# Performance work log

Measured on AMD Instinct MI355X. Metric: run time of the kernel, lower is better.

The kernel has to match this reference:

```python
import jax, jax.numpy as jnp
import numpy as np

D_MODEL = 768
D_HID = 3072
D_OUT = 768
N_EXP = 8
TOP_K = 2
B, S = 2, 2048
LN_EPS = 1e-5


def setup_inputs() -> dict:
    key = jax.random.key(0)
    ks = jax.random.split(key, 10)
    sc_in = 1.0 / np.sqrt(D_MODEL)
    sc_hid = 1.0 / np.sqrt(D_HID)
    return {
        "x": jax.random.normal(ks[0], (B, S, D_MODEL), dtype=jnp.float32),
        "Wr": jax.random.normal(ks[1], (D_MODEL, N_EXP), dtype=jnp.float32) * sc_in,
        "br": jnp.zeros((N_EXP,), dtype=jnp.float32),
        "W1": jax.random.normal(ks[2], (N_EXP, D_MODEL, D_HID), dtype=jnp.float32) * sc_in,
        "b1": jnp.zeros((N_EXP, D_HID), dtype=jnp.float32),
        "W2": jax.random.normal(ks[3], (N_EXP, D_HID, D_OUT), dtype=jnp.float32) * sc_hid,
        "b2": jnp.zeros((N_EXP, D_OUT), dtype=jnp.float32),
        "ln_g": jnp.ones((D_OUT,), dtype=jnp.float32),
        "ln_b": jnp.zeros((D_OUT,), dtype=jnp.float32),
    }


def reference(x, Wr, br, W1, b1, W2, b2, ln_g, ln_b):
    # --- top-k router ---
    logits = jnp.einsum("bsd,de->bse", x, Wr) + br          # [B,S,E]
    probs = jax.nn.softmax(logits, axis=-1)
    top_vals, top_idx = jax.lax.top_k(probs, TOP_K)          # [B,S,K]
    routing_weights = top_vals / jnp.sum(top_vals, axis=-1, keepdims=True)

    # per-token weight given to each expert (0 if not selected)
    onehot = jax.nn.one_hot(top_idx, N_EXP, dtype=x.dtype)   # [B,S,K,E]
    expert_weights = jnp.einsum("bsk,bske->bse", routing_weights, onehot)

    # --- dense per-expert FFN over ALL tokens (faithful to source loop) ---
    h = jax.nn.gelu(jnp.einsum("bsd,edh->besh", x, W1) + b1[None, :, None, :])
    y = jnp.einsum("besh,eho->beso", h, W2) + b2[None, :, None, :]  # [B,E,S,O]

    # weighted combine
    out = jnp.einsum("beso,bse->bso", y, expert_weights)     # [B,S,O]

    # --- output LayerNorm ---
    mu = jnp.mean(out, axis=-1, keepdims=True)
    var = jnp.mean(jnp.square(out - mu), axis=-1, keepdims=True)
    out = (out - mu) * jax.lax.rsqrt(var + LN_EPS) * ln_g + ln_b
    return out
```

## Files before the change

kernel.cpp:

```cpp
#include <hip/hip_runtime.h>
#include <hip/hip_bf16.h>

#define TOKENS 4096
#define DMODEL 768
#define DHID   3072
#define NEXP   8
#define MAXT   40

typedef __bf16 bf16x8 __attribute__((ext_vector_type(8)));
typedef float  f32x4  __attribute__((ext_vector_type(4)));
typedef unsigned short ushort_t;

#define VMCNT(n) asm volatile("s_waitcnt vmcnt(" #n ")" ::: "memory")

__device__ __forceinline__ void wg_barrier() {
    asm volatile("" ::: "memory");
    __builtin_amdgcn_s_barrier();
    asm volatile("" ::: "memory");
}

__device__ __forceinline__ float gelu_tanh(float x) {
    float z = 0.7978845608028654f * (x + 0.044715f * x * x * x);
    float t = 1.0f - 2.0f / (__expf(2.0f * z) + 1.0f);
    return 0.5f * x * (1.0f + t);
}

__device__ __forceinline__ float bf2f(ushort_t u) {
    unsigned v = ((unsigned)u) << 16;
    return __builtin_bit_cast(float, v);
}

__device__ __forceinline__ void gload16(const void* g, void* l) {
    __builtin_amdgcn_global_load_lds((const __attribute__((address_space(1))) void*)g,
                                     (__attribute__((address_space(3))) void*)l, 16, 0, 0);
}

__global__ void k_transpose_cvt(const float* __restrict__ in, ushort_t* __restrict__ out,
                                int R, int C) {
    __shared__ float tile[64 * 68];
    const int bx = blockIdx.x, by = blockIdx.y, bz = blockIdx.z;
    const float* ip = in + (size_t)bz * R * C;
    ushort_t* op = out + (size_t)bz * R * C;
    const int tid = threadIdx.x;
    {
        const int cq = tid & 15, rg = tid >> 4;
#pragma unroll
        for (int i = 0; i < 4; ++i) {
            int rl = rg + i * 16;
            float4 v = *(const float4*)(ip + (size_t)(by * 64 + rl) * C + bx * 64 + cq * 4);
            *(float4*)(&tile[rl * 68 + cq * 4]) = v;
        }
    }
    __syncthreads();
    {
        const int rq = tid & 15, cg = tid >> 4;
#pragma unroll
        for (int i = 0; i < 4; ++i) {
            int cl = cg + i * 16;
            ushort4 o;
            o.x = __builtin_bit_cast(ushort_t, (__bf16)tile[(rq * 4 + 0) * 68 + cl]);
            o.y = __builtin_bit_cast(ushort_t, (__bf16)tile[(rq * 4 + 1) * 68 + cl]);
            o.z = __builtin_bit_cast(ushort_t, (__bf16)tile[(rq * 4 + 2) * 68 + cl]);
            o.w = __builtin_bit_cast(ushort_t, (__bf16)tile[(rq * 4 + 3) * 68 + cl]);
            *(ushort4*)(op + (size_t)(bx * 64 + cl) * R + by * 64 + rq * 4) = o;
        }
    }
}

__launch_bounds__(256)
__global__ void k_router(const float* __restrict__ x, const float* __restrict__ Wr,
                         const float* __restrict__ br, int* __restrict__ cnt,
                         int* __restrict__ tok, int* __restrict__ slot,
                         float* __restrict__ wslot, ushort_t* __restrict__ xb) {
    __shared__ float WrT[NEXP * DMODEL];
    __shared__ int   te0[32], te1[32];
    __shared__ int   lcnt[NEXP], gbase[NEXP];

    const int tid = threadIdx.x;
    const int wv = tid >> 6, lane = tid & 63;

#pragma unroll
    for (int i = 0; i < 6; ++i) {
        int idx4 = i * 256 + tid;
        float4 v = ((const float4*)Wr)[idx4];
        int flat = idx4 * 4;
        int d = flat >> 3, e0 = flat & 7;
        WrT[(e0 + 0) * DMODEL + d] = v.x;
        WrT[(e0 + 1) * DMODEL + d] = v.y;
        WrT[(e0 + 2) * DMODEL + d] = v.z;
        WrT[(e0 + 3) * DMODEL + d] = v.w;
    }
    if (tid < NEXP) lcnt[tid] = 0;
    float brv[8];
#pragma unroll
    for (int e = 0; e < 8; ++e) brv[e] = br[e];
    __syncthreads();

#pragma unroll 1
    for (int it = 0; it < 8; ++it) {
        int t = blockIdx.x * 32 + wv * 8 + it;
        const float* xr = x + (size_t)t * DMODEL;
        float4 xv[3];
#pragma unroll
        for (int j = 0; j < 3; ++j) xv[j] = *(const float4*)(xr + (j * 64 + lane) * 4);
#pragma unroll
        for (int j = 0; j < 3; ++j) {
            int base = (j * 64 + lane) * 4;
            ushort4 o;
            o.x = __builtin_bit_cast(ushort_t, (__bf16)xv[j].x);
            o.y = __builtin_bit_cast(ushort_t, (__bf16)xv[j].y);
            o.z = __builtin_bit_cast(ushort_t, (__bf16)xv[j].z);
            o.w = __builtin_bit_cast(ushort_t, (__bf16)xv[j].w);
            *(ushort4*)(xb + (size_t)t * DMODEL + base) = o;
        }
        float lg[8];
#pragma unroll
        for (int e = 0; e < 8; ++e) {
            float s = 0.f;
#pragma unroll
            for (int j = 0; j < 3; ++j) {
                const float4 wv4 = *(const float4*)(&WrT[e * DMODEL + (j * 64 + lane) * 4]);
                s += xv[j].x * wv4.x;
                s += xv[j].y * wv4.y;
                s += xv[j].z * wv4.z;
                s += xv[j].w * wv4.w;
            }
#pragma unroll
            for (int o = 32; o > 0; o >>= 1) s += __shfl_xor(s, o);
            lg[e] = s + brv[e];
        }
        if (lane == 0) {
            int e0 = 0; float b0 = lg[0];
#pragma unroll
            for (int e = 1; e < 8; ++e) if (lg[e] > b0) { b0 = lg[e]; e0 = e; }
            int e1 = -1; float b1v = -1e30f;
#pragma unroll
            for (int e = 0; e < 8; ++e) if (e != e0 && lg[e] > b1v) { b1v = lg[e]; e1 = e; }
            float w0 = 1.f / (1.f + __expf(b1v - b0));
            float w1 = 1.f - w0;
            int lt = wv * 8 + it;
            te0[lt] = e0; te1[lt] = e1;
            wslot[2 * t] = w0; wslot[2 * t + 1] = w1;
        }
    }
    __syncthreads();

    int myE = 0, myPos = 0, myTok = 0, myK = 0;
    if (tid < 64) {
        int lt = tid >> 1; myK = tid & 1;
        myE = myK ? te1[lt] : te0[lt];
        myTok = blockIdx.x * 32 + lt;
        myPos = atomicAdd(&lcnt[myE], 1);
    }
    __syncthreads();
    if (tid < NEXP) gbase[tid] = atomicAdd(&cnt[tid], lcnt[tid]);
    __syncthreads();
    if (tid < 64) {
        int g = gbase[myE] + myPos;
        tok[myE * TOKENS + g] = myTok;
        slot[myE * TOKENS + g] = 2 * myTok + myK;
    }
}

__global__ void k_sched(const int* __restrict__ cnt, int* __restrict__ sch) {
    if (threadIdx.x == 0) {
        int base = 0, n = 0;
        for (int e = 0; e < NEXP; ++e) {
            sch[2 + e] = base;
            int ce = cnt[e];
            for (int m = 0; m < ce; m += 256) sch[16 + n++] = (e << 20) | m;
            base += ce;
        }
        sch[0] = n;
    }
}


#define ISSUE(c, kt1, BOFF)                                                            \
    {                                                                                  \
        _Pragma("unroll")                                                              \
        for (int i_ = 0; i_ < 2; ++i_) {                                               \
            const ushort_t* s_ = (((c) & 1) ? bPtr[i_] : aPtr[i_]) + (kt1) * 64 + (((c) >> 1) * 32); \
            gload16(s_, ldsB + (BOFF) + (((c) & 1) ? 32768 : 0) + (((c) >> 1) * 16384) \
                            + w * 2048 + i_ * 1024);                                   \
        }                                                                              \
    }

#define MFMA32                                                                         \
    __builtin_amdgcn_s_setprio(1);                                                     \
    _Pragma("unroll")                                                                  \
    for (int mi = 0; mi < 8; ++mi) {                                                   \
        _Pragma("unroll")                                                              \
        for (int ni = 0; ni < 4; ++ni)                                                 \
            acc[mi][ni] = __builtin_amdgcn_mfma_f32_16x16x32_bf16(af[mi], bf[ni], acc[mi][ni], 0, 0, 0); \
    }                                                                                  \
    __builtin_amdgcn_s_setprio(0);

#define TILE2(kt, BUFOFF, PF, LAST)                                                    \
    {                                                                                  \
        const char* bufL = ldsB + (BUFOFF);                                            \
        bf16x8 af[8], bf[4];                                                           \
                                                  \
        _Pragma("unroll")                                                              \
        for (int mi = 0; mi < 8; ++mi) af[mi] = *(const bf16x8*)(bufL + abase + mi * 1024); \
        _Pragma("unroll")                                                              \
        for (int ni = 0; ni < 4; ++ni) bf[ni] = *(const bf16x8*)(bufL + bbase + ni * 1024); \
        if (PF) { ISSUE(0, (kt) + 1, (BUFOFF) ^ 65536) ISSUE(1, (kt) + 1, (BUFOFF) ^ 65536) } \
        if (LAST) { VMCNT(0); } else { VMCNT(4); }                                     \
        wg_barrier();                                                                  \
        MFMA32                                                                         \
        wg_barrier();                                                                  \
                                                  \
        _Pragma("unroll")                                                              \
        for (int mi = 0; mi < 8; ++mi) af[mi] = *(const bf16x8*)(bufL + abase + 16384 + mi * 1024); \
        _Pragma("unroll")                                                              \
        for (int ni = 0; ni < 4; ++ni) bf[ni] = *(const bf16x8*)(bufL + bbase + 16384 + ni * 1024); \
        if (PF) { ISSUE(2, (kt) + 1, (BUFOFF) ^ 65536) ISSUE(3, (kt) + 1, (BUFOFF) ^ 65536) \
                  VMCNT(4); }                                                          \
        else    { VMCNT(0); }                                                          \
        wg_barrier();                                                                  \
        MFMA32                                                                         \
        wg_barrier();                                                                  \
    }

template<bool STAGE1>
__launch_bounds__(512, 1)
__global__ void k_gemm8(const ushort_t* __restrict__ Abase, const int* __restrict__ tok,
                        const int* __restrict__ slot, const ushort_t* __restrict__ Wb,
                        const float* __restrict__ bias, void* __restrict__ outp,
                        const int* __restrict__ cnt, const int* __restrict__ sch) {
    constexpr int KR  = STAGE1 ? DMODEL : DHID;
    constexpr int NCn = STAGE1 ? DHID : DMODEL;
    constexpr int NT  = STAGE1 ? (DMODEL / 64) : (DHID / 2 / 64);

    const int bx = blockIdx.x;
    const int tile = (bx & 7) * 5 + (bx >> 3);
    const int nT = sch[0];
    if (tile >= nT) return;
    const int ent = sch[16 + tile];
    const int e = ent >> 20, m0 = ent & 0xFFFFF;
    const int ce = cnt[e];
    const int bH = sch[2 + e];
    const int n0 = blockIdx.y * 256;
    const int kbase = STAGE1 ? 0 : (int)blockIdx.z * (DHID / 2);

    __shared__ ushort_t lds[65536];
    char* ldsB = (char*)lds;

    const int tid = threadIdx.x, lane = tid & 63, w = tid >> 6;
    const int wm = w >> 2, wn = w & 3;
    const int wmBase = wm * 128, wnBase = wn * 64;
    const int fr = lane & 15, fg = lane >> 4;

    const ushort_t* aPtr[2];
    const ushort_t* bPtr[2];
#pragma unroll
    for (int i = 0; i < 2; ++i) {
        int j = w * 2 + i;
        int row = j * 16 + (lane >> 2);
        int gblk = (lane & 3) ^ ((row >> 1) & 3);
        int gi = min(m0 + row, ce - 1);
        size_t ar = STAGE1 ? (size_t)tok[e * TOKENS + gi] : (size_t)(bH + gi);
        aPtr[i] = Abase + ar * KR + kbase + gblk * 8;
        bPtr[i] = Wb + ((size_t)e * NCn + n0 + row) * KR + kbase + gblk * 8;
    }

    const int arow0 = wmBase + fr;
    const int abase = arow0 * 64 + ((fg ^ ((arow0 >> 1) & 3)) << 4);
    const int brow0 = wnBase + fr;
    const int bbase = 32768 + brow0 * 64 + ((fg ^ ((brow0 >> 1) & 3)) << 4);

    f32x4 acc[8][4] = {};

    ISSUE(0, 0, 0) ISSUE(1, 0, 0) ISSUE(2, 0, 0) ISSUE(3, 0, 0)
    VMCNT(4);
    wg_barrier();

#pragma unroll 1
    for (int kt = 0; kt < NT - 2; kt += 2) {
        TILE2(kt, 0, 1, 0)
        TILE2(kt + 1, 65536, 1, 0)
    }
    TILE2(NT - 2, 0, 1, 0)
    TILE2(NT - 1, 65536, 0, 1)

    float bv[4];
#pragma unroll
    for (int ni = 0; ni < 4; ++ni)
        bv[ni] = bias[e * NCn + n0 + wnBase + ni * 16 + fr];
#pragma unroll
    for (int mi = 0; mi < 8; ++mi) {
#pragma unroll
        for (int r4 = 0; r4 < 4; ++r4) {
            int gi = m0 + wmBase + mi * 16 + fg * 4 + r4;
            if (gi < ce) {
                if constexpr (STAGE1) {
                    size_t orow = (size_t)(bH + gi);
#pragma unroll
                    for (int ni = 0; ni < 4; ++ni) {
                        int col = n0 + wnBase + ni * 16 + fr;
                        float v = gelu_tanh(acc[mi][ni][r4] + bv[ni]);
                        ((ushort_t*)outp)[orow * DHID + col] =
                            __builtin_bit_cast(ushort_t, (__bf16)v);
                    }
                } else {
                    size_t orow = (size_t)blockIdx.z * 8192 + (size_t)slot[e * TOKENS + gi];
                    float badd = (blockIdx.z == 0) ? 1.f : 0.f;
#pragma unroll
                    for (int ni = 0; ni < 4; ++ni) {
                        int col = n0 + wnBase + ni * 16 + fr;
                        float v = acc[mi][ni][r4] + badd * bv[ni];
                        ((ushort_t*)outp)[orow * DMODEL + col] =
                            __builtin_bit_cast(ushort_t, (__bf16)v);
                    }
                }
            }
        }
    }
}

__global__ void k_ln(const ushort_t* __restrict__ Y2, const float* __restrict__ wslot,
                     const float* __restrict__ g, const float* __restrict__ b,
                     float* __restrict__ out) {
    int wv = threadIdx.x >> 6, lane = threadIdx.x & 63;
    int t = blockIdx.x * 4 + wv;
    const ushort_t* r00 = Y2 + (size_t)(2 * t) * DMODEL;
    const ushort_t* r01 = Y2 + (size_t)(8192 + 2 * t) * DMODEL;
    const ushort_t* r10 = r00 + DMODEL;
    const ushort_t* r11 = r01 + DMODEL;
    float w0 = wslot[2 * t], w1 = wslot[2 * t + 1];
    float4 v[3];
    float s = 0.f, ss = 0.f;
#pragma unroll
    for (int j = 0; j < 3; ++j) {
        int base = (j * 64 + lane) * 4;
        ushort4 a0 = *(const ushort4*)(r00 + base);
        ushort4 a1 = *(const ushort4*)(r01 + base);
        ushort4 c0 = *(const ushort4*)(r10 + base);
        ushort4 c1 = *(const ushort4*)(r11 + base);
        float4 c;
        c.x = w0 * (bf2f(a0.x) + bf2f(a1.x)) + w1 * (bf2f(c0.x) + bf2f(c1.x));
        c.y = w0 * (bf2f(a0.y) + bf2f(a1.y)) + w1 * (bf2f(c0.y) + bf2f(c1.y));
        c.z = w0 * (bf2f(a0.z) + bf2f(a1.z)) + w1 * (bf2f(c0.z) + bf2f(c1.z));
        c.w = w0 * (bf2f(a0.w) + bf2f(a1.w)) + w1 * (bf2f(c0.w) + bf2f(c1.w));
        v[j] = c;
        s  += c.x + c.y + c.z + c.w;
        ss += c.x * c.x + c.y * c.y + c.z * c.z + c.w * c.w;
    }
#pragma unroll
    for (int o = 32; o > 0; o >>= 1) { s += __shfl_xor(s, o); ss += __shfl_xor(ss, o); }
    float mu = s * (1.f / 768.f);
    float var = ss * (1.f / 768.f) - mu * mu;
    float inv = rsqrtf(var + 1e-5f);
    float* row = out + (size_t)t * DMODEL;
#pragma unroll
    for (int j = 0; j < 3; ++j) {
        int base = (j * 64 + lane) * 4;
        float4 gv = *(const float4*)(g + base);
        float4 bv = *(const float4*)(b + base);
        float4 o4;
        o4.x = (v[j].x - mu) * inv * gv.x + bv.x;
        o4.y = (v[j].y - mu) * inv * gv.y + bv.y;
        o4.z = (v[j].z - mu) * inv * gv.z + bv.z;
        o4.w = (v[j].w - mu) * inv * gv.w + bv.w;
        *(float4*)(row + base) = o4;
    }
}

extern "C" void kernel_launch(void* const* d_in, const int* in_sizes, int n_in,
                              void* d_out, int out_size, void* d_ws, size_t ws_size,
                              hipStream_t stream) {
    const float* x    = (const float*)d_in[0];
    const float* Wr   = (const float*)d_in[1];
    const float* br   = (const float*)d_in[2];
    const float* W1   = (const float*)d_in[3];
    const float* b1   = (const float*)d_in[4];
    const float* W2   = (const float*)d_in[5];
    const float* b2   = (const float*)d_in[6];
    const float* ln_g = (const float*)d_in[7];
    const float* ln_b = (const float*)d_in[8];
    float* out = (float*)d_out;

    char* ws = (char*)d_ws;
    int*      cnt   = (int*)(ws + 0);
    int*      sch   = (int*)(ws + 64);
    int*      tok   = (int*)(ws + 4096);
    int*      slot  = (int*)(ws + 135168);
    float*    wslot = (float*)(ws + 266240);
    ushort_t* xb    = (ushort_t*)(ws + 327680);
    ushort_t* W1t   = (ushort_t*)(ws + 6619136);
    ushort_t* W2t   = (ushort_t*)(ws + 44367872);
    ushort_t* H     = (ushort_t*)(ws + 82116608);
    ushort_t* Y2    = (ushort_t*)(ws + 132448256);

    hipMemsetAsync(cnt, 0, 32, stream);

    k_transpose_cvt<<<dim3(DHID / 64, DMODEL / 64, NEXP), dim3(256), 0, stream>>>(W1, W1t, DMODEL, DHID);
    k_transpose_cvt<<<dim3(DMODEL / 64, DHID / 64, NEXP), dim3(256), 0, stream>>>(W2, W2t, DHID, DMODEL);
    k_router<<<dim3(TOKENS / 32), dim3(256), 0, stream>>>(x, Wr, br, cnt, tok, slot, wslot, xb);
    k_sched<<<dim3(1), dim3(64), 0, stream>>>(cnt, sch);

    k_gemm8<true><<<dim3(MAXT, DHID / 256, 1), dim3(512), 0, stream>>>(
        xb, tok, slot, W1t, b1, H, cnt, sch);
    k_gemm8<false><<<dim3(MAXT, DMODEL / 256, 2), dim3(512), 0, stream>>>(
        H, tok, slot, W2t, b2, Y2, cnt, sch);

    k_ln<<<dim3(TOKENS / 4), dim3(256), 0, stream>>>(Y2, wslot, ln_g, ln_b, out);
}
```

Before: 204.1 us.

## Shrink grouped-GEMM tiles to 128x128 with 256 threads and two blocks per CU

Halves the GEMM block tile from 256x256 to 128x128, uses 4 waves instead of 8, and allows two workgroups per CU. The scheduler now emits 128-row tiles, so MAXT grows to cover the extra tiles. The K-loop is rewritten as a simpler double-buffered loop with one wait per iteration instead of split half-tile prefetches. The intent is more blocks and less padding waste on the ragged expert token counts. The cost is lower data reuse per tile, more global traffic, and a less finely overlapped pipeline.

```diff
diff --git a/kernel.cpp b/kernel.cpp
--- a/kernel.cpp
+++ b/kernel.cpp
@@ -5,7 +5,7 @@
 #define DMODEL 768
 #define DHID   3072
 #define NEXP   8
-#define MAXT   40
+#define MAXT   72
 
 typedef __bf16 bf16x8 __attribute__((ext_vector_type(8)));
 typedef float  f32x4  __attribute__((ext_vector_type(4)));
@@ -168,63 +168,15 @@
         for (int e = 0; e < NEXP; ++e) {
             sch[2 + e] = base;
             int ce = cnt[e];
-            for (int m = 0; m < ce; m += 256) sch[16 + n++] = (e << 20) | m;
+            for (int m = 0; m < ce; m += 128) sch[16 + n++] = (e << 20) | m;
             base += ce;
         }
         sch[0] = n;
     }
 }
 
-
-#define ISSUE(c, kt1, BOFF)                                                            \
-    {                                                                                  \
-        _Pragma("unroll")                                                              \
-        for (int i_ = 0; i_ < 2; ++i_) {                                               \
-            const ushort_t* s_ = (((c) & 1) ? bPtr[i_] : aPtr[i_]) + (kt1) * 64 + (((c) >> 1) * 32); \
-            gload16(s_, ldsB + (BOFF) + (((c) & 1) ? 32768 : 0) + (((c) >> 1) * 16384) \
-                            + w * 2048 + i_ * 1024);                                   \
-        }                                                                              \
-    }
-
-#define MFMA32                                                                         \
-    __builtin_amdgcn_s_setprio(1);                                                     \
-    _Pragma("unroll")                                                                  \
-    for (int mi = 0; mi < 8; ++mi) {                                                   \
-        _Pragma("unroll")                                                              \
-        for (int ni = 0; ni < 4; ++ni)                                                 \
-            acc[mi][ni] = __builtin_amdgcn_mfma_f32_16x16x32_bf16(af[mi], bf[ni], acc[mi][ni], 0, 0, 0); \
-    }                                                                                  \
-    __builtin_amdgcn_s_setprio(0);
-
-#define TILE2(kt, BUFOFF, PF, LAST)                                                    \
-    {                                                                                  \
-        const char* bufL = ldsB + (BUFOFF);                                            \
-        bf16x8 af[8], bf[4];                                                           \
-                                                  \
-        _Pragma("unroll")                                                              \
-        for (int mi = 0; mi < 8; ++mi) af[mi] = *(const bf16x8*)(bufL + abase + mi * 1024); \
-        _Pragma("unroll")                                                              \
-        for (int ni = 0; ni < 4; ++ni) bf[ni] = *(const bf16x8*)(bufL + bbase + ni * 1024); \
-        if (PF) { ISSUE(0, (kt) + 1, (BUFOFF) ^ 65536) ISSUE(1, (kt) + 1, (BUFOFF) ^ 65536) } \
-        if (LAST) { VMCNT(0); } else { VMCNT(4); }                                     \
-        wg_barrier();                                                                  \
-        MFMA32                                                                         \
-        wg_barrier();                                                                  \
-                                                  \
-        _Pragma("unroll")                                                              \
-        for (int mi = 0; mi < 8; ++mi) af[mi] = *(const bf16x8*)(bufL + abase + 16384 + mi * 1024); \
-        _Pragma("unroll")                                                              \
-        for (int ni = 0; ni < 4; ++ni) bf[ni] = *(const bf16x8*)(bufL + bbase + 16384 + ni * 1024); \
-        if (PF) { ISSUE(2, (kt) + 1, (BUFOFF) ^ 65536) ISSUE(3, (kt) + 1, (BUFOFF) ^ 65536) \
-                  VMCNT(4); }                                                          \
-        else    { VMCNT(0); }                                                          \
-        wg_barrier();                                                                  \
-        MFMA32                                                                         \
-        wg_barrier();                                                                  \
-    }
-
 template<bool STAGE1>
-__launch_bounds__(512, 1)
+__launch_bounds__(256, 2)
 __global__ void k_gemm8(const ushort_t* __restrict__ Abase, const int* __restrict__ tok,
                         const int* __restrict__ slot, const ushort_t* __restrict__ Wb,
                         const float* __restrict__ bias, void* __restrict__ outp,
@@ -234,30 +186,29 @@
     constexpr int NT  = STAGE1 ? (DMODEL / 64) : (DHID / 2 / 64);
 
     const int bx = blockIdx.x;
-    const int tile = (bx & 7) * 5 + (bx >> 3);
+    const int tile = (bx & 7) * 9 + (bx >> 3);
     const int nT = sch[0];
     if (tile >= nT) return;
     const int ent = sch[16 + tile];
     const int e = ent >> 20, m0 = ent & 0xFFFFF;
     const int ce = cnt[e];
     const int bH = sch[2 + e];
-    const int n0 = blockIdx.y * 256;
+    const int n0 = blockIdx.y * 128;
     const int kbase = STAGE1 ? 0 : (int)blockIdx.z * (DHID / 2);
 
-    __shared__ ushort_t lds[65536];
+    __shared__ ushort_t lds[32768];
     char* ldsB = (char*)lds;
 
     const int tid = threadIdx.x, lane = tid & 63, w = tid >> 6;
-    const int wm = w >> 2, wn = w & 3;
-    const int wmBase = wm * 128, wnBase = wn * 64;
+    const int wm = w >> 1, wn = w & 1;
+    const int wmBase = wm * 64, wnBase = wn * 64;
     const int fr = lane & 15, fg = lane >> 4;
 
     const ushort_t* aPtr[2];
     const ushort_t* bPtr[2];
 #pragma unroll
     for (int i = 0; i < 2; ++i) {
-        int j = w * 2 + i;
-        int row = j * 16 + (lane >> 2);
+        int row = (w * 2 + i) * 16 + (lane >> 2);
         int gblk = (lane & 3) ^ ((row >> 1) & 3);
         int gi = min(m0 + row, ce - 1);
         size_t ar = STAGE1 ? (size_t)tok[e * TOKENS + gi] : (size_t)(bH + gi);
@@ -265,31 +216,66 @@
         bPtr[i] = Wb + ((size_t)e * NCn + n0 + row) * KR + kbase + gblk * 8;
     }
 
+    auto stage4 = [&](int kt1, int boff) {
+#pragma unroll
+        for (int i = 0; i < 2; ++i) {
+            const ushort_t* a = aPtr[i] + kt1 * 64;
+            const ushort_t* b = bPtr[i] + kt1 * 64;
+            gload16(a,      ldsB + boff +         w * 2048 + i * 1024);
+            gload16(a + 32, ldsB + boff +  8192 + w * 2048 + i * 1024);
+            gload16(b,      ldsB + boff + 16384 + w * 2048 + i * 1024);
+            gload16(b + 32, ldsB + boff + 24576 + w * 2048 + i * 1024);
+        }
+    };
+
     const int arow0 = wmBase + fr;
     const int abase = arow0 * 64 + ((fg ^ ((arow0 >> 1) & 3)) << 4);
     const int brow0 = wnBase + fr;
-    const int bbase = 32768 + brow0 * 64 + ((fg ^ ((brow0 >> 1) & 3)) << 4);
-
-    f32x4 acc[8][4] = {};
-
-    ISSUE(0, 0, 0) ISSUE(1, 0, 0) ISSUE(2, 0, 0) ISSUE(3, 0, 0)
-    VMCNT(4);
+    const int bbase = 16384 + brow0 * 64 + ((fg ^ ((brow0 >> 1) & 3)) << 4);
+
+    f32x4 acc[4][4] = {};
+
+    stage4(0, 0);
+    VMCNT(0);
     wg_barrier();
 
 #pragma unroll 1
-    for (int kt = 0; kt < NT - 2; kt += 2) {
-        TILE2(kt, 0, 1, 0)
-        TILE2(kt + 1, 65536, 1, 0)
-    }
-    TILE2(NT - 2, 0, 1, 0)
-    TILE2(NT - 1, 65536, 0, 1)
+    for (int kt = 0; kt < NT; ++kt) {
+        const int boff = (kt & 1) * 32768;
+        const char* bufL = ldsB + boff;
+        if (kt + 1 < NT) stage4(kt + 1, boff ^ 32768);
+
+        bf16x8 a0[4], b0[4], a1[4], b1f[4];
+#pragma unroll
+        for (int i = 0; i < 4; ++i) {
+            a0[i]  = *(const bf16x8*)(bufL + abase + i * 1024);
+            b0[i]  = *(const bf16x8*)(bufL + bbase + i * 1024);
+            a1[i]  = *(const bf16x8*)(bufL + abase + 8192 + i * 1024);
+            b1f[i] = *(const bf16x8*)(bufL + bbase + 8192 + i * 1024);
+        }
+        __builtin_amdgcn_s_setprio(1);
+#pragma unroll
+        for (int mi = 0; mi < 4; ++mi)
+#pragma unroll
+            for (int ni = 0; ni < 4; ++ni)
+                acc[mi][ni] = __builtin_amdgcn_mfma_f32_16x16x32_bf16(a0[mi], b0[ni], acc[mi][ni], 0, 0, 0);
+#pragma unroll
+        for (int mi = 0; mi < 4; ++mi)
+#pragma unroll
+            for (int ni = 0; ni < 4; ++ni)
+                acc[mi][ni] = __builtin_amdgcn_mfma_f32_16x16x32_bf16(a1[mi], b1f[ni], acc[mi][ni], 0, 0, 0);
+        __builtin_amdgcn_s_setprio(0);
+
+        VMCNT(0);
+        wg_barrier();
+    }
 
     float bv[4];
 #pragma unroll
     for (int ni = 0; ni < 4; ++ni)
         bv[ni] = bias[e * NCn + n0 + wnBase + ni * 16 + fr];
 #pragma unroll
-    for (int mi = 0; mi < 8; ++mi) {
+    for (int mi = 0; mi < 4; ++mi) {
 #pragma unroll
         for (int r4 = 0; r4 < 4; ++r4) {
             int gi = m0 + wmBase + mi * 16 + fg * 4 + r4;
@@ -400,9 +386,9 @@
     k_router<<<dim3(TOKENS / 32), dim3(256), 0, stream>>>(x, Wr, br, cnt, tok, slot, wslot, xb);
     k_sched<<<dim3(1), dim3(64), 0, stream>>>(cnt, sch);
 
-    k_gemm8<true><<<dim3(MAXT, DHID / 256, 1), dim3(512), 0, stream>>>(
+    k_gemm8<true><<<dim3(MAXT, DHID / 128, 1), dim3(256), 0, stream>>>(
         xb, tok, slot, W1t, b1, H, cnt, sch);
-    k_gemm8<false><<<dim3(MAXT, DMODEL / 256, 2), dim3(512), 0, stream>>>(
+    k_gemm8<false><<<dim3(MAXT, DMODEL / 128, 2), dim3(256), 0, stream>>>(
         H, tok, slot, W2t, b2, Y2, cnt, sch);
 
     k_ln<<<dim3(TOKENS / 4), dim3(256), 0, stream>>>(Y2, wslot, ln_g, ln_b, out);
```

Measured after the change: 208.0 us. About the same (+1.9%).

## Restructure GEMM mainloop into four finer phases with two-tile-ahead prefetch

Applied to the files above, without the earlier changes.

Replaces the two-half-tile schedule with four phases per k-tile. Each phase runs 16 MFMAs on one half of the M rows and one k-slice. Global-to-LDS staging is spread across the phases and issued up to two tiles ahead, with vmcnt(6), so more loads are in flight while MFMAs run. The B fragments are reused across both M halves and LDS addresses are precomputed per thread. In exchange there are more barriers per tile and a tighter hazard pattern, which risks overwriting a buffer still being read or waiting on the wrong load count.

```diff
diff --git a/kernel.cpp b/kernel.cpp
--- a/kernel.cpp
+++ b/kernel.cpp
@@ -176,50 +176,43 @@
 }
 
 
-#define ISSUE(c, kt1, BOFF)                                                            \
+#define STAGEH(h, t)                                                                   \
     {                                                                                  \
+        const int _ks = (h) & 1, _b = (h) >> 1;                                        \
+        const ushort_t* _s0 = (_b ? bSrc[0] : aSrc[0]) + (t) * 64 + _ks * 32;          \
+        const ushort_t* _s1 = (_b ? bSrc[1] : aSrc[1]) + (t) * 64 + _ks * 32;          \
+        char* _d = ldsB + ((t) & 1) * 65536 + _b * 32768 + _ks * 16384;                \
+        gload16(_s0, _d + tid * 16);                                                   \
+        gload16(_s1, _d + 8192 + tid * 16);                                            \
+    }
+
+#define PHASE(kt, J, KS, MH, LASTT)                                                    \
+    {                                                                                  \
+        const char* bufc = ldsB + ((kt) & 1) * 65536;                                  \
+        bf16x8 af[4];                                                                  \
         _Pragma("unroll")                                                              \
-        for (int i_ = 0; i_ < 2; ++i_) {                                               \
-            const ushort_t* s_ = (((c) & 1) ? bPtr[i_] : aPtr[i_]) + (kt1) * 64 + (((c) >> 1) * 32); \
-            gload16(s_, ldsB + (BOFF) + (((c) & 1) ? 32768 : 0) + (((c) >> 1) * 16384) \
-                            + w * 2048 + i_ * 1024);                                   \
+        for (int _m = 0; _m < 4; ++_m)                                                 \
+            af[_m] = *(const bf16x8*)(bufc + (KS) * 16384 + aoff[(MH) * 4 + _m]);      \
+        if ((MH) == 0) {                                                               \
+            _Pragma("unroll")                                                          \
+            for (int _n = 0; _n < 4; ++_n)                                             \
+                bcur[_n] = *(const bf16x8*)(bufc + 32768 + (KS) * 16384 + boff[_n]);   \
         }                                                                              \
-    }
-
-#define MFMA32                                                                         \
-    __builtin_amdgcn_s_setprio(1);                                                     \
-    _Pragma("unroll")                                                                  \
-    for (int mi = 0; mi < 8; ++mi) {                                                   \
+        if ((J) == 0) { if ((kt) >= 1 && (kt) + 1 < NT) STAGEH(1, (kt) + 1) }          \
+        else if ((J) == 1) { if ((kt) + 2 < NT) STAGEH(2, (kt) + 2) }                  \
+        else if ((J) == 2) { if ((kt) + 2 < NT) STAGEH(0, (kt) + 2) }                  \
+        else               { if ((kt) + 2 < NT) STAGEH(3, (kt) + 2) }                  \
+        if ((LASTT) && (J) == 3) { VMCNT(0); } else { VMCNT(6); }                      \
+        wg_barrier();                                                                  \
+        __builtin_amdgcn_s_setprio(1);                                                 \
         _Pragma("unroll")                                                              \
-        for (int ni = 0; ni < 4; ++ni)                                                 \
-            acc[mi][ni] = __builtin_amdgcn_mfma_f32_16x16x32_bf16(af[mi], bf[ni], acc[mi][ni], 0, 0, 0); \
-    }                                                                                  \
-    __builtin_amdgcn_s_setprio(0);
-
-#define TILE2(kt, BUFOFF, PF, LAST)                                                    \
-    {                                                                                  \
-        const char* bufL = ldsB + (BUFOFF);                                            \
-        bf16x8 af[8], bf[4];                                                           \
-                                                  \
-        _Pragma("unroll")                                                              \
-        for (int mi = 0; mi < 8; ++mi) af[mi] = *(const bf16x8*)(bufL + abase + mi * 1024); \
-        _Pragma("unroll")                                                              \
-        for (int ni = 0; ni < 4; ++ni) bf[ni] = *(const bf16x8*)(bufL + bbase + ni * 1024); \
-        if (PF) { ISSUE(0, (kt) + 1, (BUFOFF) ^ 65536) ISSUE(1, (kt) + 1, (BUFOFF) ^ 65536) } \
-        if (LAST) { VMCNT(0); } else { VMCNT(4); }                                     \
-        wg_barrier();                                                                  \
-        MFMA32                                                                         \
-        wg_barrier();                                                                  \
-                                                  \
-        _Pragma("unroll")                                                              \
-        for (int mi = 0; mi < 8; ++mi) af[mi] = *(const bf16x8*)(bufL + abase + 16384 + mi * 1024); \
-        _Pragma("unroll")                                                              \
-        for (int ni = 0; ni < 4; ++ni) bf[ni] = *(const bf16x8*)(bufL + bbase + 16384 + ni * 1024); \
-        if (PF) { ISSUE(2, (kt) + 1, (BUFOFF) ^ 65536) ISSUE(3, (kt) + 1, (BUFOFF) ^ 65536) \
-                  VMCNT(4); }                                                          \
-        else    { VMCNT(0); }                                                          \
-        wg_barrier();                                                                  \
-        MFMA32                                                                         \
+        for (int _m = 0; _m < 4; ++_m) {                                               \
+            _Pragma("unroll")                                                          \
+            for (int _n = 0; _n < 4; ++_n)                                             \
+                acc[(MH) * 4 + _m][_n] = __builtin_amdgcn_mfma_f32_16x16x32_bf16(      \
+                    af[_m], bcur[_n], acc[(MH) * 4 + _m][_n], 0, 0, 0);                \
+        }                                                                              \
+        __builtin_amdgcn_s_setprio(0);                                                 \
         wg_barrier();                                                                  \
     }
 
@@ -249,56 +242,67 @@
 
     const int tid = threadIdx.x, lane = tid & 63, w = tid >> 6;
     const int wm = w >> 2, wn = w & 3;
-    const int wmBase = wm * 128, wnBase = wn * 64;
     const int fr = lane & 15, fg = lane >> 4;
 
-    const ushort_t* aPtr[2];
-    const ushort_t* bPtr[2];
+    const ushort_t* aSrc[2];
+    const ushort_t* bSrc[2];
 #pragma unroll
     for (int i = 0; i < 2; ++i) {
-        int j = w * 2 + i;
-        int row = j * 16 + (lane >> 2);
-        int gblk = (lane & 3) ^ ((row >> 1) & 3);
+        int s = i * 512 + tid;
+        int row = s >> 2;
+        int blk = (s & 3) ^ ((row >> 1) & 3);
         int gi = min(m0 + row, ce - 1);
         size_t ar = STAGE1 ? (size_t)tok[e * TOKENS + gi] : (size_t)(bH + gi);
-        aPtr[i] = Abase + ar * KR + kbase + gblk * 8;
-        bPtr[i] = Wb + ((size_t)e * NCn + n0 + row) * KR + kbase + gblk * 8;
-    }
-
-    const int arow0 = wmBase + fr;
-    const int abase = arow0 * 64 + ((fg ^ ((arow0 >> 1) & 3)) << 4);
-    const int brow0 = wnBase + fr;
-    const int bbase = 32768 + brow0 * 64 + ((fg ^ ((brow0 >> 1) & 3)) << 4);
+        aSrc[i] = Abase + ar * KR + kbase + blk * 8;
+        bSrc[i] = Wb + ((size_t)e * NCn + n0 + row) * KR + kbase + blk * 8;
+    }
+
+    int aoff[8], boff[4];
+#pragma unroll
+    for (int mi = 0; mi < 8; ++mi) {
+        int row = wm * 128 + mi * 16 + fr;
+        aoff[mi] = row * 64 + ((fg ^ ((row >> 1) & 3)) << 4);
+    }
+#pragma unroll
+    for (int ni = 0; ni < 4; ++ni) {
+        int row = wn * 64 + ni * 16 + fr;
+        boff[ni] = row * 64 + ((fg ^ ((row >> 1) & 3)) << 4);
+    }
 
     f32x4 acc[8][4] = {};
-
-    ISSUE(0, 0, 0) ISSUE(1, 0, 0) ISSUE(2, 0, 0) ISSUE(3, 0, 0)
-    VMCNT(4);
+    bf16x8 bcur[4];
+
+#pragma unroll
+    for (int h = 0; h < 4; ++h) STAGEH(h, 0)
+#pragma unroll
+    for (int h = 0; h < 4; ++h) STAGEH(h, 1)
+    VMCNT(6);
     wg_barrier();
 
 #pragma unroll 1
-    for (int kt = 0; kt < NT - 2; kt += 2) {
-        TILE2(kt, 0, 1, 0)
-        TILE2(kt + 1, 65536, 1, 0)
-    }
-    TILE2(NT - 2, 0, 1, 0)
-    TILE2(NT - 1, 65536, 0, 1)
+    for (int kt = 0; kt < NT; ++kt) {
+        const bool lastt = (kt == NT - 2);
+        PHASE(kt, 0, 0, 0, lastt)
+        PHASE(kt, 1, 0, 1, lastt)
+        PHASE(kt, 2, 1, 0, lastt)
+        PHASE(kt, 3, 1, 1, lastt)
+    }
 
     float bv[4];
 #pragma unroll
     for (int ni = 0; ni < 4; ++ni)
-        bv[ni] = bias[e * NCn + n0 + wnBase + ni * 16 + fr];
+        bv[ni] = bias[e * NCn + n0 + wn * 64 + ni * 16 + fr];
 #pragma unroll
     for (int mi = 0; mi < 8; ++mi) {
 #pragma unroll
         for (int r4 = 0; r4 < 4; ++r4) {
-            int gi = m0 + wmBase + mi * 16 + fg * 4 + r4;
+            int gi = m0 + wm * 128 + mi * 16 + fg * 4 + r4;
             if (gi < ce) {
                 if constexpr (STAGE1) {
                     size_t orow = (size_t)(bH + gi);
 #pragma unroll
                     for (int ni = 0; ni < 4; ++ni) {
-                        int col = n0 + wnBase + ni * 16 + fr;
+                        int col = n0 + wn * 64 + ni * 16 + fr;
                         float v = gelu_tanh(acc[mi][ni][r4] + bv[ni]);
                         ((ushort_t*)outp)[orow * DHID + col] =
                             __builtin_bit_cast(ushort_t, (__bf16)v);
@@ -308,7 +312,7 @@
                     float badd = (blockIdx.z == 0) ? 1.f : 0.f;
 #pragma unroll
                     for (int ni = 0; ni < 4; ++ni) {
-                        int col = n0 + wnBase + ni * 16 + fr;
+                        int col = n0 + wn * 64 + ni * 16 + fr;
                         float v = acc[mi][ni][r4] + badd * bv[ni];
                         ((ushort_t*)outp)[orow * DMODEL + col] =
                             __builtin_bit_cast(ushort_t, (__bf16)v);
```

New measurement: 207.9 us. About the same (+1.9%).
